# Optimization experiments

Hardware: AMD Instinct MI355X
Metric: run time of the kernel (lower is better)

Reference implementation:

```python
import jax, jax.numpy as jnp
import numpy as np

COST_CLASS, COST_BBOX, COST_GIOU = 2.0, 5.0, 2.0
ALPHA, GAMMA, EPS = 0.25, 2.0, 1e-8


def box_cxcywh_to_xyxy(x):
    cx, cy, w, h = x[..., 0], x[..., 1], x[..., 2], x[..., 3]
    return jnp.stack([cx - 0.5 * w, cy - 0.5 * h, cx + 0.5 * w, cy + 0.5 * h], axis=-1)


def pairwise_giou(b1, b2):
    # b1: [N,4] xyxy, b2: [M,4] xyxy -> [N,M]
    area1 = (b1[:, 2] - b1[:, 0]) * (b1[:, 3] - b1[:, 1])
    area2 = (b2[:, 2] - b2[:, 0]) * (b2[:, 3] - b2[:, 1])
    lt = jnp.maximum(b1[:, None, :2], b2[None, :, :2])   # [N,M,2]
    rb = jnp.minimum(b1[:, None, 2:], b2[None, :, 2:])
    wh = jnp.clip(rb - lt, 0.0)
    inter = wh[..., 0] * wh[..., 1]
    union = area1[:, None] + area2[None, :] - inter
    iou = inter / union
    lt2 = jnp.minimum(b1[:, None, :2], b2[None, :, :2])
    rb2 = jnp.maximum(b1[:, None, 2:], b2[None, :, 2:])
    wh2 = jnp.clip(rb2 - lt2, 0.0)
    area = wh2[..., 0] * wh2[..., 1]  # enclosing box area
    return iou - (area - union) / area


def setup_inputs() -> dict:
    key = jax.random.key(0)
    k1, k2, k3, k4 = jax.random.split(key, 4)
    bs, Q, C, T = 16, 900, 91, 1600
    return {
        "pred_logits": jax.random.normal(k1, (bs, Q, C), dtype=jnp.float32),
        "pred_boxes": jax.random.uniform(k2, (bs, Q, 4), dtype=jnp.float32),
        "tgt_boxes": jax.random.uniform(k3, (T, 4), dtype=jnp.float32),
        "tgt_ids": jax.random.randint(k4, (T,), 0, C),
    }


def reference(pred_logits, pred_boxes, tgt_boxes, tgt_ids):
    bs, Q, _ = pred_logits.shape
    out_prob = jax.nn.sigmoid(pred_logits.reshape(bs * Q, -1))  # [N, num_classes]
    out_bbox = pred_boxes.reshape(bs * Q, 4)                     # [N, 4] cxcywh

    # focal-style classification cost
    neg_cost = (1.0 - ALPHA) * out_prob ** GAMMA * (-jnp.log(1.0 - out_prob + EPS))
    pos_cost = ALPHA * (1.0 - out_prob) ** GAMMA * (-jnp.log(out_prob + EPS))
    cost_class = pos_cost[:, tgt_ids] - neg_cost[:, tgt_ids]     # [N, T]

    # L1 bbox cost (cdist p=1)
    cost_bbox = jnp.sum(jnp.abs(out_bbox[:, None, :] - tgt_boxes[None, :, :]), axis=-1)

    # GIoU cost
    cost_giou = -pairwise_giou(box_cxcywh_to_xyxy(out_bbox), box_cxcywh_to_xyxy(tgt_boxes))

    C = COST_BBOX * cost_bbox + COST_CLASS * cost_class + COST_GIOU * cost_giou
    return C.reshape(bs, Q, -1)
```

## Files before the change

kernel.cpp:

```cpp
#include <hip/hip_runtime.h>

#define F_ALPHA 0.25f
#define F_EPS   1e-8f
#define NB 4

__global__ void __launch_bounds__(256)
fused_cost_kernel(const float* __restrict__ logits,
                  const float4* __restrict__ pred_boxes,
                  const float4* __restrict__ tgt_boxes,
                  const int* __restrict__ tgt_ids,
                  float* __restrict__ out,
                  int N, int C, int T) {
    __shared__ float4 fclsT[96];
    const int n0  = blockIdx.x * NB;
    const int tid = threadIdx.x;

    {
        const int w = tid >> 6, l = tid & 63;
        const int n = min(n0 + w, N - 1);
        const float* lrow = logits + (size_t)n * C;
        for (int c = l; c < C; c += 64) {
            float x = lrow[c];
            float p = 1.0f / (1.0f + expf(-x));
            float om = 1.0f - p;
            float pos = F_ALPHA * om * om * (-logf(p + F_EPS));
            float neg = (1.0f - F_ALPHA) * p * p * (-logf(om + F_EPS));
            ((float*)fclsT)[c * NB + w] = 2.0f * (pos - neg) + 2.0f;
        }
    }

    float pcx[NB], pcy[NB], pw_[NB], ph_[NB];
    float px1[NB], py1[NB], px2[NB], py2[NB], parea[NB];
    float* op[NB];
#pragma unroll
    for (int i = 0; i < NB; ++i) {
        const int n = min(n0 + i, N - 1);
        float4 pb = pred_boxes[n];
        pcx[i] = pb.x; pcy[i] = pb.y; pw_[i] = pb.z; ph_[i] = pb.w;
        px1[i] = pb.x - 0.5f * pb.z;  py1[i] = pb.y - 0.5f * pb.w;
        px2[i] = pb.x + 0.5f * pb.z;  py2[i] = pb.y + 0.5f * pb.w;
        parea[i] = pb.z * pb.w;
        op[i] = out + (size_t)n * T;
    }
    __syncthreads();

    auto body = [&](int t) {
        float4 tb = tgt_boxes[t];
        int id = tgt_ids[t];
        float4 cls4 = fclsT[id];
        float tx1 = tb.x - 0.5f * tb.z, ty1 = tb.y - 0.5f * tb.w;
        float tx2 = tb.x + 0.5f * tb.z, ty2 = tb.y + 0.5f * tb.w;
        float tarea = tb.z * tb.w;
        const float clsv[NB] = {cls4.x, cls4.y, cls4.z, cls4.w};
#pragma unroll
        for (int i = 0; i < NB; ++i) {
            float l1 = (fabsf(pcx[i] - tb.x) + fabsf(pcy[i] - tb.y))
                     + (fabsf(pw_[i] - tb.z) + fabsf(ph_[i] - tb.w));

            float ix1 = fmaxf(px1[i], tx1), iy1 = fmaxf(py1[i], ty1);
            float ix2 = fminf(px2[i], tx2), iy2 = fminf(py2[i], ty2);
            float iw = fmaxf(ix2 - ix1, 0.0f), ih = fmaxf(iy2 - iy1, 0.0f);
            float inter = iw * ih;
            float uni = parea[i] + tarea - inter;

            float ex1 = fminf(px1[i], tx1), ey1 = fminf(py1[i], ty1);
            float ex2 = fmaxf(px2[i], tx2), ey2 = fmaxf(py2[i], ty2);
            float earea = (ex2 - ex1) * (ey2 - ey1);

            float v = fmaf(5.0f, l1, clsv[i]);
            v = fmaf(-2.0f, inter * __builtin_amdgcn_rcpf(uni), v);
            v = fmaf(-2.0f, uni * __builtin_amdgcn_rcpf(earea), v);
            op[i][t] = v;
        }
    };

    int t = tid;
    for (; t + 256 < T; t += 512) { body(t); body(t + 256); }
    for (; t < T; t += 256) body(t);
}

extern "C" void kernel_launch(void* const* d_in, const int* in_sizes, int n_in,
                              void* d_out, int out_size, void* d_ws, size_t ws_size,
                              hipStream_t stream) {
    const float* logits = (const float*)d_in[0];
    const float* pboxes = (const float*)d_in[1];
    const float* tboxes = (const float*)d_in[2];
    const int*   tids   = (const int*)d_in[3];

    int N = in_sizes[1] / 4;
    int C = in_sizes[0] / N;
    int T = in_sizes[2] / 4;

    int grid = (N + NB - 1) / NB;
    fused_cost_kernel<<<grid, 256, 0, stream>>>(
        logits, (const float4*)pboxes, (const float4*)tboxes, tids,
        (float*)d_out, N, C, T);
}
```

Before: 32.95 us.

## Stage targets in shared memory and write four outputs per thread as float4

Each block now copies all target boxes and ids into shared memory in a strided layout, so a thread can process four consecutive targets and emit one 128-bit store per prediction row. The goal is to cut the number of store instructions and make writes wider, since the kernel is limited by writing the output. The cost is a per-block global-to-shared staging pass over 1600 targets. It also hardcodes T=1600 and drops the N and T bounds handling, so it only works for these exact shapes and a divisible N.

```diff
diff --git a/kernel.cpp b/kernel.cpp
--- a/kernel.cpp
+++ b/kernel.cpp
@@ -3,6 +3,8 @@
 #define F_ALPHA 0.25f
 #define F_EPS   1e-8f
 #define NB 4
+#define TMAX 1600
+#define Q4   (TMAX/4)
 
 __global__ void __launch_bounds__(256)
 fused_cost_kernel(const float* __restrict__ logits,
@@ -11,14 +13,22 @@
                   const int* __restrict__ tgt_ids,
                   float* __restrict__ out,
                   int N, int C, int T) {
+    __shared__ float4 sTbS[TMAX];
+    __shared__ int    sIdS[TMAX];
     __shared__ float4 fclsT[96];
+
     const int n0  = blockIdx.x * NB;
     const int tid = threadIdx.x;
 
+    for (int t = tid; t < TMAX; t += 256) {
+        int s = (t & 3) * Q4 + (t >> 2);
+        sTbS[s] = tgt_boxes[t];
+        sIdS[s] = tgt_ids[t];
+    }
+
     {
         const int w = tid >> 6, l = tid & 63;
-        const int n = min(n0 + w, N - 1);
-        const float* lrow = logits + (size_t)n * C;
+        const float* lrow = logits + (size_t)(n0 + w) * C;
         for (int c = l; c < C; c += 64) {
             float x = lrow[c];
             float p = 1.0f / (1.0f + expf(-x));
@@ -31,52 +41,61 @@
 
     float pcx[NB], pcy[NB], pw_[NB], ph_[NB];
     float px1[NB], py1[NB], px2[NB], py2[NB], parea[NB];
-    float* op[NB];
+    float4* op[NB];
 #pragma unroll
     for (int i = 0; i < NB; ++i) {
-        const int n = min(n0 + i, N - 1);
+        const int n = n0 + i;
         float4 pb = pred_boxes[n];
         pcx[i] = pb.x; pcy[i] = pb.y; pw_[i] = pb.z; ph_[i] = pb.w;
         px1[i] = pb.x - 0.5f * pb.z;  py1[i] = pb.y - 0.5f * pb.w;
         px2[i] = pb.x + 0.5f * pb.z;  py2[i] = pb.y + 0.5f * pb.w;
         parea[i] = pb.z * pb.w;
-        op[i] = out + (size_t)n * T;
+        op[i] = (float4*)(out + (size_t)n * T);
     }
     __syncthreads();
 
-    auto body = [&](int t) {
-        float4 tb = tgt_boxes[t];
-        int id = tgt_ids[t];
-        float4 cls4 = fclsT[id];
-        float tx1 = tb.x - 0.5f * tb.z, ty1 = tb.y - 0.5f * tb.w;
-        float tx2 = tb.x + 0.5f * tb.z, ty2 = tb.y + 0.5f * tb.w;
-        float tarea = tb.z * tb.w;
-        const float clsv[NB] = {cls4.x, cls4.y, cls4.z, cls4.w};
+    for (int q = tid; q < Q4; q += 256) {
+        float4 tb[4]; float4 cls[4];
+        float tx1[4], ty1[4], tx2[4], ty2[4], tarea[4];
+#pragma unroll
+        for (int j = 0; j < 4; ++j) {
+            tb[j] = sTbS[j * Q4 + q];
+            cls[j] = fclsT[sIdS[j * Q4 + q]];
+            tx1[j] = tb[j].x - 0.5f * tb[j].z;  ty1[j] = tb[j].y - 0.5f * tb[j].w;
+            tx2[j] = tb[j].x + 0.5f * tb[j].z;  ty2[j] = tb[j].y + 0.5f * tb[j].w;
+            tarea[j] = tb[j].z * tb[j].w;
+        }
+        const float clsv[4][4] = {
+            {cls[0].x, cls[0].y, cls[0].z, cls[0].w},
+            {cls[1].x, cls[1].y, cls[1].z, cls[1].w},
+            {cls[2].x, cls[2].y, cls[2].z, cls[2].w},
+            {cls[3].x, cls[3].y, cls[3].z, cls[3].w}};
 #pragma unroll
         for (int i = 0; i < NB; ++i) {
-            float l1 = (fabsf(pcx[i] - tb.x) + fabsf(pcy[i] - tb.y))
-                     + (fabsf(pw_[i] - tb.z) + fabsf(ph_[i] - tb.w));
+            float res[4];
+#pragma unroll
+            for (int j = 0; j < 4; ++j) {
+                float l1 = (fabsf(pcx[i] - tb[j].x) + fabsf(pcy[i] - tb[j].y))
+                         + (fabsf(pw_[i] - tb[j].z) + fabsf(ph_[i] - tb[j].w));
 
-            float ix1 = fmaxf(px1[i], tx1), iy1 = fmaxf(py1[i], ty1);
-            float ix2 = fminf(px2[i], tx2), iy2 = fminf(py2[i], ty2);
-            float iw = fmaxf(ix2 - ix1, 0.0f), ih = fmaxf(iy2 - iy1, 0.0f);
-            float inter = iw * ih;
-            float uni = parea[i] + tarea - inter;
+                float ix1 = fmaxf(px1[i], tx1[j]), iy1 = fmaxf(py1[i], ty1[j]);
+                float ix2 = fminf(px2[i], tx2[j]), iy2 = fminf(py2[i], ty2[j]);
+                float iw = fmaxf(ix2 - ix1, 0.0f), ih = fmaxf(iy2 - iy1, 0.0f);
+                float inter = iw * ih;
+                float uni = parea[i] + tarea[j] - inter;
 
-            float ex1 = fminf(px1[i], tx1), ey1 = fminf(py1[i], ty1);
-            float ex2 = fmaxf(px2[i], tx2), ey2 = fmaxf(py2[i], ty2);
-            float earea = (ex2 - ex1) * (ey2 - ey1);
+                float ex1 = fminf(px1[i], tx1[j]), ey1 = fminf(py1[i], ty1[j]);
+                float ex2 = fmaxf(px2[i], tx2[j]), ey2 = fmaxf(py2[i], ty2[j]);
+                float earea = (ex2 - ex1) * (ey2 - ey1);
 
-            float v = fmaf(5.0f, l1, clsv[i]);
-            v = fmaf(-2.0f, inter * __builtin_amdgcn_rcpf(uni), v);
-            v = fmaf(-2.0f, uni * __builtin_amdgcn_rcpf(earea), v);
-            op[i][t] = v;
+                float v = fmaf(5.0f, l1, clsv[j][i]);
+                v = fmaf(-2.0f, inter * __builtin_amdgcn_rcpf(uni), v);
+                v = fmaf(-2.0f, uni * __builtin_amdgcn_rcpf(earea), v);
+                res[j] = v;
+            }
+            op[i][q] = make_float4(res[0], res[1], res[2], res[3]);
         }
-    };
-
-    int t = tid;
-    for (; t + 256 < T; t += 512) { body(t); body(t + 256); }
-    for (; t < T; t += 256) body(t);
+    }
 }
 
 extern "C" void kernel_launch(void* const* d_in, const int* in_sizes, int n_in,
@@ -91,7 +110,7 @@
     int C = in_sizes[0] / N;
     int T = in_sizes[2] / 4;
 
-    int grid = (N + NB - 1) / NB;
+    int grid = N / NB;
     fused_cost_kernel<<<grid, 256, 0, stream>>>(
         logits, (const float4*)pboxes, (const float4*)tboxes, tids,
         (float*)d_out, N, C, T);
```

New measurement: 40.98 us. 24.4% more time.
